# Performance work log

Measured on AMD Instinct MI355X. Metric: run time of the kernel, lower is better.

The kernel has to match this reference:

```python
import jax, jax.numpy as jnp
import numpy as np

N, E, EQ, DIM = 50000, 800000, 100000, 256


def setup_inputs() -> dict:
    key = jax.random.key(0)
    k1, k2, k3, k4, k5 = jax.random.split(key, 5)
    edges = jax.random.randint(k1, (2, EQ), 0, N)
    adj_row = jax.random.randint(k2, (E,), 0, N)
    adj_col = jax.random.randint(k3, (E,), 0, N)
    node_weight = jax.random.uniform(k4, (N,), dtype=jnp.float32)
    # torchhd-style bipolar hypervectors scaled by sqrt(1/dim)
    scale = (1.0 / DIM) ** 0.5
    node_vectors = jnp.sign(jax.random.normal(k5, (N, DIM), dtype=jnp.float32)) * scale
    return dict(edges=edges, adj_row=adj_row, adj_col=adj_col,
                node_weight=node_weight, node_vectors=node_vectors)


def reference(edges, adj_row, adj_col, node_weight, node_vectors):
    n = node_vectors.shape[0]
    # get_random_node_vectors: embedding * node_weight
    x = node_vectors * node_weight[:, None]                       # [N, dim]
    # one_hop_x = A @ x ; two_hop_x = A @ one_hop_x (binary adjacency)
    one_hop = jax.ops.segment_sum(x[adj_col], adj_row, num_segments=n)       # [N, dim]
    two_hop = jax.ops.segment_sum(one_hop[adj_col], adj_row, num_segments=n)  # [N, dim]
    deg = jax.ops.segment_sum(jnp.ones(adj_row.shape, x.dtype), adj_row, num_segments=n)  # [N]
    s, t = edges[0], edges[1]
    dot = lambda a, b: (a * b).sum(-1)
    count_1_1 = dot(one_hop[s], one_hop[t])
    count_1_2 = dot(one_hop[s], two_hop[t]) + dot(two_hop[s], one_hop[t])
    count_2_2 = dot(two_hop[s] - deg[s][:, None] * x[s],
                    two_hop[t] - deg[t][:, None] * x[t])
    count_self_1_2 = dot(one_hop[s], two_hop[s]) + dot(one_hop[t], two_hop[t])
    return (count_1_1, count_1_2, count_2_2, count_self_1_2)
```

## Files before the change

kernel.cpp:

```cpp
#include <hip/hip_runtime.h>

#define DIM 256
#define NODE_U2 192
#define NODE_U4 96
#define SLOT_OH_U4 32
#define SLOT_TH_U4 64

#define NSL 8
#define ECAP 2048

__device__ __forceinline__ unsigned int f2bf_rne(float f) {
    unsigned int u = __float_as_uint(f);
    return (u + 0x7fffu + ((u >> 16) & 1u)) >> 16;
}
__device__ __forceinline__ float bf_lo(unsigned int u) {
    return __uint_as_float(u << 16);
}
__device__ __forceinline__ float bf_hi(unsigned int u) {
    return __uint_as_float(u & 0xffff0000u);
}
__device__ __forceinline__ unsigned int pack2(float a, float b) {
    return f2bf_rne(a) | (f2bf_rne(b) << 16);
}

#define ACC8(v)                                            \
    do {                                                   \
        a0 += bf_lo((v).x); a1 += bf_hi((v).x);            \
        a2 += bf_lo((v).y); a3 += bf_hi((v).y);            \
        a4 += bf_lo((v).z); a5 += bf_hi((v).z);            \
        a6 += bf_lo((v).w); a7 += bf_hi((v).w);            \
    } while (0)

__global__ void x_kernel(const float* __restrict__ nv,
                         const float* __restrict__ w,
                         uint2* __restrict__ cmb,
                         uint2* __restrict__ xs_sl,
                         int total_u2, int N) {
    int i0 = blockIdx.x * blockDim.x + threadIdx.x;
    int stride = gridDim.x * blockDim.x;
    for (int i = i0; i < total_u2; i += stride) {
        float4 v = reinterpret_cast<const float4*>(nv)[i];
        int node = i >> 6;
        int j = i & 63;
        float wt = w[node];
        uint2 r;
        r.x = pack2(v.x * wt, v.y * wt);
        r.y = pack2(v.z * wt, v.w * wt);
        cmb[(size_t)node * NODE_U2 + j] = r;
        int s = j >> 3;
        xs_sl[((size_t)s * N + node) * 8 + (j & 7)] = r;
    }
}

__global__ void hist_kernel(const int* __restrict__ adj_row,
                            int* __restrict__ cnt, int E, int per_part) {
    int bp = blockIdx.x & 7;
    unsigned lo = (unsigned)(bp * per_part);
    int chunk = blockIdx.x >> 3;
    int nchunks = gridDim.x >> 3;
    int E4 = E >> 2;
    for (int i = chunk * 256 + threadIdx.x; i < E4; i += nchunks * 256) {
        int4 r4 = reinterpret_cast<const int4*>(adj_row)[i];
        if ((unsigned)(r4.x - lo) < (unsigned)per_part) atomicAdd(&cnt[r4.x], 1);
        if ((unsigned)(r4.y - lo) < (unsigned)per_part) atomicAdd(&cnt[r4.y], 1);
        if ((unsigned)(r4.z - lo) < (unsigned)per_part) atomicAdd(&cnt[r4.z], 1);
        if ((unsigned)(r4.w - lo) < (unsigned)per_part) atomicAdd(&cnt[r4.w], 1);
    }
    if (bp == 0 && chunk == 0) {
        for (int e = (E & ~3) + threadIdx.x; e < E; e += 256)
            atomicAdd(&cnt[adj_row[e]], 1);
    }
}

__global__ void block_sum_kernel(const int* __restrict__ in,
                                 int* __restrict__ sums, int n) {
    __shared__ int lds[256];
    int i = blockIdx.x * 256 + threadIdx.x;
    lds[threadIdx.x] = (i < n) ? in[i] : 0;
    __syncthreads();
    #pragma unroll
    for (int off = 128; off > 0; off >>= 1) {
        if (threadIdx.x < off) lds[threadIdx.x] += lds[threadIdx.x + off];
        __syncthreads();
    }
    if (threadIdx.x == 0) sums[blockIdx.x] = lds[0];
}

__global__ void scan_sums_kernel(int* __restrict__ sums, int nb,
                                 int* __restrict__ total_out) {
    __shared__ int lds[256];
    int v = (threadIdx.x < nb) ? sums[threadIdx.x] : 0;
    lds[threadIdx.x] = v;
    __syncthreads();
    #pragma unroll
    for (int off = 1; off < 256; off <<= 1) {
        int t = (threadIdx.x >= off) ? lds[threadIdx.x - off] : 0;
        __syncthreads();
        lds[threadIdx.x] += t;
        __syncthreads();
    }
    if (threadIdx.x < nb) sums[threadIdx.x] = lds[threadIdx.x] - v;
    if (threadIdx.x == 255) *total_out = lds[255];
}

__global__ void scan_block_kernel(const int* __restrict__ in,
                                  const int* __restrict__ sums,
                                  int* __restrict__ out1,
                                  int* __restrict__ out2, int n) {
    __shared__ int lds[256];
    int i = blockIdx.x * 256 + threadIdx.x;
    int v = (i < n) ? in[i] : 0;
    lds[threadIdx.x] = v;
    __syncthreads();
    #pragma unroll
    for (int off = 1; off < 256; off <<= 1) {
        int t = (threadIdx.x >= off) ? lds[threadIdx.x - off] : 0;
        __syncthreads();
        lds[threadIdx.x] += t;
        __syncthreads();
    }
    if (i < n) {
        int excl = sums[blockIdx.x] + lds[threadIdx.x] - v;
        out1[i] = excl;
        out2[i] = excl;
    }
}

__global__ void scatter_perm_part_kernel(const int* __restrict__ row,
                                         const int* __restrict__ col,
                                         int* __restrict__ cursor,
                                         unsigned short* __restrict__ perm,
                                         int E, int per_part) {
    int bp = blockIdx.x & 7;
    unsigned lo = (unsigned)(bp * per_part);
    int chunk = blockIdx.x >> 3;
    int nchunks = gridDim.x >> 3;
    int E4 = E >> 2;
    for (int i = chunk * 256 + threadIdx.x; i < E4; i += nchunks * 256) {
        int4 r4 = reinterpret_cast<const int4*>(row)[i];
        int e = i << 2;
        if ((unsigned)(r4.x - lo) < (unsigned)per_part) {
            int pos = atomicAdd(&cursor[r4.x], 1);
            perm[pos] = (unsigned short)col[e];
        }
        if ((unsigned)(r4.y - lo) < (unsigned)per_part) {
            int pos = atomicAdd(&cursor[r4.y], 1);
            perm[pos] = (unsigned short)col[e + 1];
        }
        if ((unsigned)(r4.z - lo) < (unsigned)per_part) {
            int pos = atomicAdd(&cursor[r4.z], 1);
            perm[pos] = (unsigned short)col[e + 2];
        }
        if ((unsigned)(r4.w - lo) < (unsigned)per_part) {
            int pos = atomicAdd(&cursor[r4.w], 1);
            perm[pos] = (unsigned short)col[e + 3];
        }
    }
    if (bp == 0 && chunk == 0) {
        for (int e = (E & ~3) + threadIdx.x; e < E; e += 256) {
            int pos = atomicAdd(&cursor[row[e]], 1);
            perm[pos] = (unsigned short)col[e];
        }
    }
}

__global__ void gather_sliced_kernel(const int* __restrict__ row_ptr,
                                     const unsigned short* __restrict__ perm,
                                     const uint4* __restrict__ src_sl,
                                     uint4* __restrict__ dst_sl,
                                     uint4* __restrict__ dst_cmb_slot,
                                     int N) {
    __shared__ unsigned short eidx[ECAP];
    int s = blockIdx.x & (NSL - 1);
    int rb = blockIdx.x >> 3;
    int r0 = rb * 64;
    int rlim = r0 + 64 < N ? r0 + 64 : N;
    int beg0 = row_ptr[r0];
    int end0 = row_ptr[rlim];
    int L = end0 - beg0;
    int Lc = L < ECAP ? L : ECAP;
    for (int i = threadIdx.x; i < Lc; i += 256) eidx[i] = perm[beg0 + i];
    __syncthreads();

    int g = threadIdx.x >> 2;
    int j = threadIdx.x & 3;
    int r = r0 + g;
    if (r >= N) return;

    int beg = row_ptr[r];
    int end = row_ptr[r + 1];
    const uint4* base = src_sl + (size_t)s * N * 4;

    float a0 = 0.f, a1 = 0.f, a2 = 0.f, a3 = 0.f;
    float a4 = 0.f, a5 = 0.f, a6 = 0.f, a7 = 0.f;

    if (end - beg0 <= ECAP) {
        int o = beg - beg0;
        int cnt = end - beg;
        int k = 0;
        for (; k + 3 < cnt; k += 4) {
            int c0 = eidx[o + k];
            int c1 = eidx[o + k + 1];
            int c2 = eidx[o + k + 2];
            int c3 = eidx[o + k + 3];
            uint4 v0 = base[(size_t)c0 * 4 + j];
            uint4 v1 = base[(size_t)c1 * 4 + j];
            uint4 v2 = base[(size_t)c2 * 4 + j];
            uint4 v3 = base[(size_t)c3 * 4 + j];
            ACC8(v0); ACC8(v1); ACC8(v2); ACC8(v3);
        }
        for (; k < cnt; ++k) {
            uint4 v = base[(size_t)eidx[o + k] * 4 + j];
            ACC8(v);
        }
    } else {
        for (int e = beg; e < end; ++e) {
            uint4 v = base[(size_t)perm[e] * 4 + j];
            ACC8(v);
        }
    }

    uint4 o4;
    o4.x = pack2(a0, a1);
    o4.y = pack2(a2, a3);
    o4.z = pack2(a4, a5);
    o4.w = pack2(a6, a7);
    if (dst_sl) dst_sl[((size_t)s * N + r) * 4 + j] = o4;
    dst_cmb_slot[(size_t)r * NODE_U4 + s * 4 + j] = o4;
}

__global__ void query_kernel(const int* __restrict__ es,
                             const int* __restrict__ et,
                             const uint4* __restrict__ cmb4,
                             const int* __restrict__ row_ptr,
                             float* __restrict__ out, int nq) {
    int gid = blockIdx.x * blockDim.x + threadIdx.x;
    int q = gid >> 5;
    if (q >= nq) return;
    int l = gid & 31;

    int s = es[q];
    int t = et[q];

    const uint4* ns = cmb4 + (size_t)s * NODE_U4;
    const uint4* nt = cmb4 + (size_t)t * NODE_U4;

    uint4 vxs = ns[l];
    uint4 vos = ns[SLOT_OH_U4 + l];
    uint4 vts = ns[SLOT_TH_U4 + l];
    uint4 vxt = nt[l];
    uint4 vot = nt[SLOT_OH_U4 + l];
    uint4 vtt = nt[SLOT_TH_U4 + l];
    float ds = (float)(row_ptr[s + 1] - row_ptr[s]);
    float dt = (float)(row_ptr[t + 1] - row_ptr[t]);

    float c11 = 0.f, c12 = 0.f, c22 = 0.f, cs = 0.f;
    const unsigned int* pxs = (const unsigned int*)&vxs;
    const unsigned int* pxt = (const unsigned int*)&vxt;
    const unsigned int* pos_ = (const unsigned int*)&vos;
    const unsigned int* pot = (const unsigned int*)&vot;
    const unsigned int* pts = (const unsigned int*)&vts;
    const unsigned int* ptt = (const unsigned int*)&vtt;
    #pragma unroll
    for (int k = 0; k < 4; ++k) {
        {
            float fxs = bf_lo(pxs[k]), fxt = bf_lo(pxt[k]);
            float fos = bf_lo(pos_[k]), fot = bf_lo(pot[k]);
            float fts = bf_lo(pts[k]), ftt = bf_lo(ptt[k]);
            c11 += fos * fot;
            c12 += fos * ftt + fts * fot;
            float as = fts - ds * fxs;
            float bt = ftt - dt * fxt;
            c22 += as * bt;
            cs  += fos * fts + fot * ftt;
        }
        {
            float fxs = bf_hi(pxs[k]), fxt = bf_hi(pxt[k]);
            float fos = bf_hi(pos_[k]), fot = bf_hi(pot[k]);
            float fts = bf_hi(pts[k]), ftt = bf_hi(ptt[k]);
            c11 += fos * fot;
            c12 += fos * ftt + fts * fot;
            float as = fts - ds * fxs;
            float bt = ftt - dt * fxt;
            c22 += as * bt;
            cs  += fos * fts + fot * ftt;
        }
    }

    #pragma unroll
    for (int off = 16; off > 0; off >>= 1) {
        c11 += __shfl_xor(c11, off);
        c12 += __shfl_xor(c12, off);
        c22 += __shfl_xor(c22, off);
        cs  += __shfl_xor(cs,  off);
    }

    if (l == 0) {
        out[q]          = c11;
        out[nq + q]     = c12;
        out[2 * nq + q] = c22;
        out[3 * nq + q] = cs;
    }
}

extern "C" void kernel_launch(void* const* d_in, const int* in_sizes, int n_in,
                              void* d_out, int out_size, void* d_ws, size_t ws_size,
                              hipStream_t stream) {
    const int*   edges        = (const int*)  d_in[0];
    const int*   adj_row      = (const int*)  d_in[1];
    const int*   adj_col      = (const int*)  d_in[2];
    const float* node_weight  = (const float*)d_in[3];
    const float* node_vectors = (const float*)d_in[4];

    const int EQ = in_sizes[0] / 2;
    const int E  = in_sizes[1];
    const int N  = in_sizes[3];

    uint2* cmb   = (uint2*)d_ws;
    uint2* xs_sl = cmb + (size_t)N * NODE_U2;
    uint2* oh_sl = xs_sl + (size_t)N * NSL * 8;
    int* row_ptr = (int*)(oh_sl + (size_t)N * NSL * 8);
    int* cursor  = row_ptr + (N + 1);
    int* cnt     = cursor + N;
    unsigned short* perm = (unsigned short*)(cnt + N);
    int* s1      = (int*)(perm + ((E + 1) & ~1));

    const int* es = edges;
    const int* et = edges + EQ;
    float* out = (float*)d_out;

    const int nb0 = (N + 255) / 256;
    const int per_part = (N + 7) / 8;

    hipMemsetAsync(cnt, 0, (size_t)N * sizeof(int), stream);
    int total_u2 = N * 64;
    x_kernel<<<2048, 256, 0, stream>>>(node_vectors, node_weight,
                                       cmb, xs_sl, total_u2, N);

    hist_kernel<<<2048, 256, 0, stream>>>(adj_row, cnt, E, per_part);

    block_sum_kernel<<<nb0, 256, 0, stream>>>(cnt, s1, N);
    scan_sums_kernel<<<1, 256, 0, stream>>>(s1, nb0, row_ptr + N);
    scan_block_kernel<<<nb0, 256, 0, stream>>>(cnt, s1, row_ptr, cursor, N);
    scatter_perm_part_kernel<<<2048, 256, 0, stream>>>(adj_row, adj_col,
                                                       cursor, perm, E,
                                                       per_part);

    const uint4* xs4 = (const uint4*)xs_sl;
    uint4* oh4 = (uint4*)oh_sl;
    uint4* cmb4 = (uint4*)cmb;
    int nrb = (N + 63) / 64;
    int gblocks = nrb * NSL;
    gather_sliced_kernel<<<gblocks, 256, 0, stream>>>(
        row_ptr, perm, xs4, oh4, cmb4 + SLOT_OH_U4, N);
    gather_sliced_kernel<<<gblocks, 256, 0, stream>>>(
        row_ptr, perm, (const uint4*)oh4, (uint4*)nullptr,
        cmb4 + SLOT_TH_U4, N);

    int qthreads = EQ * 32;
    query_kernel<<<(qthreads + 255) / 256, 256, 0, stream>>>(
        es, et, cmb4, row_ptr, out, EQ);
}
```

Baseline: 238.8 us.

## Sort rows by degree for load-balanced gather and fuse x with histogram

```diff
diff --git a/kernel.cpp b/kernel.cpp
--- a/kernel.cpp
+++ b/kernel.cpp
@@ -7,7 +7,8 @@
 #define SLOT_TH_U4 64
 
 #define NSL 8
-#define ECAP 2048
+#define ECAP 4096
+#define NBIN 64
 
 __device__ __forceinline__ unsigned int f2bf_rne(float f) {
     unsigned int u = __float_as_uint(f);
@@ -31,11 +32,13 @@
         a6 += bf_lo((v).w); a7 += bf_hi((v).w);            \
     } while (0)
 
-__global__ void x_kernel(const float* __restrict__ nv,
-                         const float* __restrict__ w,
-                         uint2* __restrict__ cmb,
-                         uint2* __restrict__ xs_sl,
-                         int total_u2, int N) {
+__global__ void x_and_hist_kernel(const float* __restrict__ nv,
+                                  const float* __restrict__ w,
+                                  uint2* __restrict__ cmb,
+                                  uint2* __restrict__ xs_sl,
+                                  int total_u2, int N,
+                                  const int* __restrict__ adj_row,
+                                  int* __restrict__ deg, int E, int per_part) {
     int i0 = blockIdx.x * blockDim.x + threadIdx.x;
     int stride = gridDim.x * blockDim.x;
     for (int i = i0; i < total_u2; i += stride) {
@@ -50,10 +53,6 @@
         int s = j >> 3;
         xs_sl[((size_t)s * N + node) * 8 + (j & 7)] = r;
     }
-}
-
-__global__ void hist_kernel(const int* __restrict__ adj_row,
-                            int* __restrict__ cnt, int E, int per_part) {
     int bp = blockIdx.x & 7;
     unsigned lo = (unsigned)(bp * per_part);
     int chunk = blockIdx.x >> 3;
@@ -61,14 +60,57 @@
     int E4 = E >> 2;
     for (int i = chunk * 256 + threadIdx.x; i < E4; i += nchunks * 256) {
         int4 r4 = reinterpret_cast<const int4*>(adj_row)[i];
-        if ((unsigned)(r4.x - lo) < (unsigned)per_part) atomicAdd(&cnt[r4.x], 1);
-        if ((unsigned)(r4.y - lo) < (unsigned)per_part) atomicAdd(&cnt[r4.y], 1);
-        if ((unsigned)(r4.z - lo) < (unsigned)per_part) atomicAdd(&cnt[r4.z], 1);
-        if ((unsigned)(r4.w - lo) < (unsigned)per_part) atomicAdd(&cnt[r4.w], 1);
+        if ((unsigned)(r4.x - lo) < (unsigned)per_part) atomicAdd(&deg[r4.x], 1);
+        if ((unsigned)(r4.y - lo) < (unsigned)per_part) atomicAdd(&deg[r4.y], 1);
+        if ((unsigned)(r4.z - lo) < (unsigned)per_part) atomicAdd(&deg[r4.z], 1);
+        if ((unsigned)(r4.w - lo) < (unsigned)per_part) atomicAdd(&deg[r4.w], 1);
     }
     if (bp == 0 && chunk == 0) {
         for (int e = (E & ~3) + threadIdx.x; e < E; e += 256)
-            atomicAdd(&cnt[adj_row[e]], 1);
+            atomicAdd(&deg[adj_row[e]], 1);
+    }
+}
+
+__global__ void bin_count_kernel(const int* __restrict__ deg,
+                                 int* __restrict__ blockBin, int n, int nblk) {
+    __shared__ int h[NBIN];
+    if (threadIdx.x < NBIN) h[threadIdx.x] = 0;
+    __syncthreads();
+    int i = blockIdx.x * 256 + threadIdx.x;
+    if (i < n) {
+        int b = deg[i]; b = b > NBIN - 1 ? NBIN - 1 : b;
+        atomicAdd(&h[b], 1);
+    }
+    __syncthreads();
+    if (threadIdx.x < NBIN)
+        blockBin[(size_t)threadIdx.x * nblk + blockIdx.x] = h[threadIdx.x];
+}
+
+__global__ void rank_assign_kernel(const int* __restrict__ deg,
+                                   const int* __restrict__ off,
+                                   int* __restrict__ rank2node,
+                                   int* __restrict__ node2rank,
+                                   int* __restrict__ degR, int n, int nblk) {
+    __shared__ int h[NBIN];
+    __shared__ int base[NBIN];
+    if (threadIdx.x < NBIN) h[threadIdx.x] = 0;
+    __syncthreads();
+    int i = blockIdx.x * 256 + threadIdx.x;
+    int b = 0, loc = 0, d = 0;
+    bool act = i < n;
+    if (act) {
+        d = deg[i]; b = d > NBIN - 1 ? NBIN - 1 : d;
+        loc = atomicAdd(&h[b], 1);
+    }
+    __syncthreads();
+    if (threadIdx.x < NBIN)
+        base[threadIdx.x] = off[(size_t)threadIdx.x * nblk + blockIdx.x];
+    __syncthreads();
+    if (act) {
+        int r = base[b] + loc;
+        rank2node[r] = i;
+        node2rank[i] = r;
+        degR[r] = d;
     }
 }
 
@@ -128,6 +170,7 @@
 
 __global__ void scatter_perm_part_kernel(const int* __restrict__ row,
                                          const int* __restrict__ col,
+                                         const int* __restrict__ node2rank,
                                          int* __restrict__ cursor,
                                          unsigned short* __restrict__ perm,
                                          int E, int per_part) {
@@ -139,26 +182,31 @@
     for (int i = chunk * 256 + threadIdx.x; i < E4; i += nchunks * 256) {
         int4 r4 = reinterpret_cast<const int4*>(row)[i];
         int e = i << 2;
-        if ((unsigned)(r4.x - lo) < (unsigned)per_part) {
-            int pos = atomicAdd(&cursor[r4.x], 1);
+        int k0 = node2rank[r4.x];
+        int k1 = node2rank[r4.y];
+        int k2 = node2rank[r4.z];
+        int k3 = node2rank[r4.w];
+        if ((unsigned)(k0 - lo) < (unsigned)per_part) {
+            int pos = atomicAdd(&cursor[k0], 1);
             perm[pos] = (unsigned short)col[e];
         }
-        if ((unsigned)(r4.y - lo) < (unsigned)per_part) {
-            int pos = atomicAdd(&cursor[r4.y], 1);
+        if ((unsigned)(k1 - lo) < (unsigned)per_part) {
+            int pos = atomicAdd(&cursor[k1], 1);
             perm[pos] = (unsigned short)col[e + 1];
         }
-        if ((unsigned)(r4.z - lo) < (unsigned)per_part) {
-            int pos = atomicAdd(&cursor[r4.z], 1);
+        if ((unsigned)(k2 - lo) < (unsigned)per_part) {
+            int pos = atomicAdd(&cursor[k2], 1);
             perm[pos] = (unsigned short)col[e + 2];
         }
-        if ((unsigned)(r4.w - lo) < (unsigned)per_part) {
-            int pos = atomicAdd(&cursor[r4.w], 1);
+        if ((unsigned)(k3 - lo) < (unsigned)per_part) {
+            int pos = atomicAdd(&cursor[k3], 1);
             perm[pos] = (unsigned short)col[e + 3];
         }
     }
     if (bp == 0 && chunk == 0) {
         for (int e = (E & ~3) + threadIdx.x; e < E; e += 256) {
-            int pos = atomicAdd(&cursor[row[e]], 1);
+            int k = node2rank[row[e]];
+            int pos = atomicAdd(&cursor[k], 1);
             perm[pos] = (unsigned short)col[e];
         }
     }
@@ -166,6 +214,7 @@
 
 __global__ void gather_sliced_kernel(const int* __restrict__ row_ptr,
                                      const unsigned short* __restrict__ perm,
+                                     const int* __restrict__ rank2node,
                                      const uint4* __restrict__ src_sl,
                                      uint4* __restrict__ dst_sl,
                                      uint4* __restrict__ dst_cmb_slot,
@@ -187,6 +236,7 @@
     int r = r0 + g;
     if (r >= N) return;
 
+    int node = rank2node[r];
     int beg = row_ptr[r];
     int end = row_ptr[r + 1];
     const uint4* base = src_sl + (size_t)s * N * 4;
@@ -194,7 +244,7 @@
     float a0 = 0.f, a1 = 0.f, a2 = 0.f, a3 = 0.f;
     float a4 = 0.f, a5 = 0.f, a6 = 0.f, a7 = 0.f;
 
-    if (end - beg0 <= ECAP) {
+    if (L <= ECAP) {
         int o = beg - beg0;
         int cnt = end - beg;
         int k = 0;
@@ -225,14 +275,14 @@
     o4.y = pack2(a2, a3);
     o4.z = pack2(a4, a5);
     o4.w = pack2(a6, a7);
-    if (dst_sl) dst_sl[((size_t)s * N + r) * 4 + j] = o4;
-    dst_cmb_slot[(size_t)r * NODE_U4 + s * 4 + j] = o4;
+    if (dst_sl) dst_sl[((size_t)s * N + node) * 4 + j] = o4;
+    dst_cmb_slot[(size_t)node * NODE_U4 + s * 4 + j] = o4;
 }
 
 __global__ void query_kernel(const int* __restrict__ es,
                              const int* __restrict__ et,
                              const uint4* __restrict__ cmb4,
-                             const int* __restrict__ row_ptr,
+                             const int* __restrict__ deg,
                              float* __restrict__ out, int nq) {
     int gid = blockIdx.x * blockDim.x + threadIdx.x;
     int q = gid >> 5;
@@ -251,8 +301,8 @@
     uint4 vxt = nt[l];
     uint4 vot = nt[SLOT_OH_U4 + l];
     uint4 vtt = nt[SLOT_TH_U4 + l];
-    float ds = (float)(row_ptr[s + 1] - row_ptr[s]);
-    float dt = (float)(row_ptr[t + 1] - row_ptr[t]);
+    float ds = (float)deg[s];
+    float dt = (float)deg[t];
 
     float c11 = 0.f, c12 = 0.f, c22 = 0.f, cs = 0.f;
     const unsigned int* pxs = (const unsigned int*)&vxs;
@@ -316,35 +366,50 @@
     const int E  = in_sizes[1];
     const int N  = in_sizes[3];
 
+    const int nbB = (N + 255) / 256;
+    const int n1  = NBIN * nbB;
+    const int nbS = (n1 + 255) / 256;
+
     uint2* cmb   = (uint2*)d_ws;
     uint2* xs_sl = cmb + (size_t)N * NODE_U2;
-    uint2* oh_sl = xs_sl + (size_t)N * NSL * 8;
-    int* row_ptr = (int*)(oh_sl + (size_t)N * NSL * 8);
-    int* cursor  = row_ptr + (N + 1);
-    int* cnt     = cursor + N;
-    unsigned short* perm = (unsigned short*)(cnt + N);
-    int* s1      = (int*)(perm + ((E + 1) & ~1));
+    uint2* oh_sl = xs_sl + (size_t)N * 64;
+    int* deg      = (int*)(oh_sl + (size_t)N * 64);
+    int* node2rank = deg + N;
+    int* rank2node = node2rank + N;
+    int* degR     = rank2node + N;
+    int* row_ptr  = degR + N;
+    int* cursor   = row_ptr + (N + 1);
+    int* blockBin = cursor + N;
+    int* s1       = blockBin + n1;
+    unsigned short* perm = (unsigned short*)(s1 + 256);
 
     const int* es = edges;
     const int* et = edges + EQ;
     float* out = (float*)d_out;
 
-    const int nb0 = (N + 255) / 256;
-    const int per_part = (N + 7) / 8;
-
-    hipMemsetAsync(cnt, 0, (size_t)N * sizeof(int), stream);
+    const int per_part_node = (N + 7) / 8;
+    const int per_part_rank = (N + 7) / 8;
+
+    hipMemsetAsync(deg, 0, (size_t)N * sizeof(int), stream);
     int total_u2 = N * 64;
-    x_kernel<<<2048, 256, 0, stream>>>(node_vectors, node_weight,
-                                       cmb, xs_sl, total_u2, N);
-
-    hist_kernel<<<2048, 256, 0, stream>>>(adj_row, cnt, E, per_part);
-
-    block_sum_kernel<<<nb0, 256, 0, stream>>>(cnt, s1, N);
-    scan_sums_kernel<<<1, 256, 0, stream>>>(s1, nb0, row_ptr + N);
-    scan_block_kernel<<<nb0, 256, 0, stream>>>(cnt, s1, row_ptr, cursor, N);
+    x_and_hist_kernel<<<2048, 256, 0, stream>>>(node_vectors, node_weight,
+                                                cmb, xs_sl, total_u2, N,
+                                                adj_row, deg, E, per_part_node);
+
+    bin_count_kernel<<<nbB, 256, 0, stream>>>(deg, blockBin, N, nbB);
+    block_sum_kernel<<<nbS, 256, 0, stream>>>(blockBin, s1, n1);
+    scan_sums_kernel<<<1, 256, 0, stream>>>(s1, nbS, cursor );
+    scan_block_kernel<<<nbS, 256, 0, stream>>>(blockBin, s1, blockBin,
+                                               blockBin, n1);
+    rank_assign_kernel<<<nbB, 256, 0, stream>>>(deg, blockBin, rank2node,
+                                                node2rank, degR, N, nbB);
+
+    block_sum_kernel<<<nbB, 256, 0, stream>>>(degR, s1, N);
+    scan_sums_kernel<<<1, 256, 0, stream>>>(s1, nbB, row_ptr + N);
+    scan_block_kernel<<<nbB, 256, 0, stream>>>(degR, s1, row_ptr, cursor, N);
     scatter_perm_part_kernel<<<2048, 256, 0, stream>>>(adj_row, adj_col,
-                                                       cursor, perm, E,
-                                                       per_part);
+                                                       node2rank, cursor, perm,
+                                                       E, per_part_rank);
 
     const uint4* xs4 = (const uint4*)xs_sl;
     uint4* oh4 = (uint4*)oh_sl;
@@ -352,12 +417,12 @@
     int nrb = (N + 63) / 64;
     int gblocks = nrb * NSL;
     gather_sliced_kernel<<<gblocks, 256, 0, stream>>>(
-        row_ptr, perm, xs4, oh4, cmb4 + SLOT_OH_U4, N);
+        row_ptr, perm, rank2node, xs4, oh4, cmb4 + SLOT_OH_U4, N);
     gather_sliced_kernel<<<gblocks, 256, 0, stream>>>(
-        row_ptr, perm, (const uint4*)oh4, (uint4*)nullptr,
+        row_ptr, perm, rank2node, (const uint4*)oh4, (uint4*)nullptr,
         cmb4 + SLOT_TH_U4, N);
 
     int qthreads = EQ * 32;
     query_kernel<<<(qthreads + 255) / 256, 256, 0, stream>>>(
-        es, et, cmb4, row_ptr, out, EQ);
-}
+        es, et, cmb4, deg, out, EQ);
+}
```

Measured after the change: 244.5 us. 2.4% more time.

## Sort queries by source node and fuse histogram into x kernel

Applied to the files above, without the earlier changes.

```diff
diff --git a/kernel.cpp b/kernel.cpp
--- a/kernel.cpp
+++ b/kernel.cpp
@@ -31,11 +31,16 @@
         a6 += bf_lo((v).w); a7 += bf_hi((v).w);            \
     } while (0)
 
-__global__ void x_kernel(const float* __restrict__ nv,
-                         const float* __restrict__ w,
-                         uint2* __restrict__ cmb,
-                         uint2* __restrict__ xs_sl,
-                         int total_u2, int N) {
+__global__ void x_and_hist_kernel(const float* __restrict__ nv,
+                                  const float* __restrict__ w,
+                                  uint2* __restrict__ cmb,
+                                  uint2* __restrict__ xs_sl,
+                                  int total_u2, int N,
+                                  const int* __restrict__ adj_row,
+                                  int* __restrict__ cnt, int E,
+                                  const int* __restrict__ es,
+                                  int* __restrict__ qcnt, int EQ,
+                                  int per_part) {
     int i0 = blockIdx.x * blockDim.x + threadIdx.x;
     int stride = gridDim.x * blockDim.x;
     for (int i = i0; i < total_u2; i += stride) {
@@ -50,10 +55,6 @@
         int s = j >> 3;
         xs_sl[((size_t)s * N + node) * 8 + (j & 7)] = r;
     }
-}
-
-__global__ void hist_kernel(const int* __restrict__ adj_row,
-                            int* __restrict__ cnt, int E, int per_part) {
     int bp = blockIdx.x & 7;
     unsigned lo = (unsigned)(bp * per_part);
     int chunk = blockIdx.x >> 3;
@@ -66,9 +67,19 @@
         if ((unsigned)(r4.z - lo) < (unsigned)per_part) atomicAdd(&cnt[r4.z], 1);
         if ((unsigned)(r4.w - lo) < (unsigned)per_part) atomicAdd(&cnt[r4.w], 1);
     }
+    int Q4 = EQ >> 2;
+    for (int i = chunk * 256 + threadIdx.x; i < Q4; i += nchunks * 256) {
+        int4 s4 = reinterpret_cast<const int4*>(es)[i];
+        if ((unsigned)(s4.x - lo) < (unsigned)per_part) atomicAdd(&qcnt[s4.x], 1);
+        if ((unsigned)(s4.y - lo) < (unsigned)per_part) atomicAdd(&qcnt[s4.y], 1);
+        if ((unsigned)(s4.z - lo) < (unsigned)per_part) atomicAdd(&qcnt[s4.z], 1);
+        if ((unsigned)(s4.w - lo) < (unsigned)per_part) atomicAdd(&qcnt[s4.w], 1);
+    }
     if (bp == 0 && chunk == 0) {
         for (int e = (E & ~3) + threadIdx.x; e < E; e += 256)
             atomicAdd(&cnt[adj_row[e]], 1);
+        for (int q = (EQ & ~3) + threadIdx.x; q < EQ; q += 256)
+            atomicAdd(&qcnt[es[q]], 1);
     }
 }
 
@@ -160,6 +171,48 @@
         for (int e = (E & ~3) + threadIdx.x; e < E; e += 256) {
             int pos = atomicAdd(&cursor[row[e]], 1);
             perm[pos] = (unsigned short)col[e];
+        }
+    }
+}
+
+__global__ void qscatter_part_kernel(const int* __restrict__ es,
+                                     const int* __restrict__ et,
+                                     int* __restrict__ qcur,
+                                     int* __restrict__ qs,
+                                     int* __restrict__ qt,
+                                     int* __restrict__ qidx,
+                                     int EQ, int per_part) {
+    int bp = blockIdx.x & 7;
+    unsigned lo = (unsigned)(bp * per_part);
+    int chunk = blockIdx.x >> 3;
+    int nchunks = gridDim.x >> 3;
+    int Q4 = EQ >> 2;
+    for (int i = chunk * 256 + threadIdx.x; i < Q4; i += nchunks * 256) {
+        int4 s4 = reinterpret_cast<const int4*>(es)[i];
+        int4 t4 = reinterpret_cast<const int4*>(et)[i];
+        int q = i << 2;
+        if ((unsigned)(s4.x - lo) < (unsigned)per_part) {
+            int pos = atomicAdd(&qcur[s4.x], 1);
+            qs[pos] = s4.x; qt[pos] = t4.x; qidx[pos] = q;
+        }
+        if ((unsigned)(s4.y - lo) < (unsigned)per_part) {
+            int pos = atomicAdd(&qcur[s4.y], 1);
+            qs[pos] = s4.y; qt[pos] = t4.y; qidx[pos] = q + 1;
+        }
+        if ((unsigned)(s4.z - lo) < (unsigned)per_part) {
+            int pos = atomicAdd(&qcur[s4.z], 1);
+            qs[pos] = s4.z; qt[pos] = t4.z; qidx[pos] = q + 2;
+        }
+        if ((unsigned)(s4.w - lo) < (unsigned)per_part) {
+            int pos = atomicAdd(&qcur[s4.w], 1);
+            qs[pos] = s4.w; qt[pos] = t4.w; qidx[pos] = q + 3;
+        }
+    }
+    if (bp == 0 && chunk == 0) {
+        for (int q = (EQ & ~3) + threadIdx.x; q < EQ; q += 256) {
+            int s = es[q];
+            int pos = atomicAdd(&qcur[s], 1);
+            qs[pos] = s; qt[pos] = et[q]; qidx[pos] = q;
         }
     }
 }
@@ -194,7 +247,7 @@
     float a0 = 0.f, a1 = 0.f, a2 = 0.f, a3 = 0.f;
     float a4 = 0.f, a5 = 0.f, a6 = 0.f, a7 = 0.f;
 
-    if (end - beg0 <= ECAP) {
+    if (L <= ECAP) {
         int o = beg - beg0;
         int cnt = end - beg;
         int k = 0;
@@ -229,18 +282,20 @@
     dst_cmb_slot[(size_t)r * NODE_U4 + s * 4 + j] = o4;
 }
 
-__global__ void query_kernel(const int* __restrict__ es,
-                             const int* __restrict__ et,
+__global__ void query_kernel(const int* __restrict__ qs,
+                             const int* __restrict__ qt,
+                             const int* __restrict__ qidx,
                              const uint4* __restrict__ cmb4,
-                             const int* __restrict__ row_ptr,
+                             const int* __restrict__ deg,
                              float* __restrict__ out, int nq) {
     int gid = blockIdx.x * blockDim.x + threadIdx.x;
     int q = gid >> 5;
     if (q >= nq) return;
     int l = gid & 31;
 
-    int s = es[q];
-    int t = et[q];
+    int s = qs[q];
+    int t = qt[q];
+    int oq = qidx[q];
 
     const uint4* ns = cmb4 + (size_t)s * NODE_U4;
     const uint4* nt = cmb4 + (size_t)t * NODE_U4;
@@ -251,8 +306,8 @@
     uint4 vxt = nt[l];
     uint4 vot = nt[SLOT_OH_U4 + l];
     uint4 vtt = nt[SLOT_TH_U4 + l];
-    float ds = (float)(row_ptr[s + 1] - row_ptr[s]);
-    float dt = (float)(row_ptr[t + 1] - row_ptr[t]);
+    float ds = (float)deg[s];
+    float dt = (float)deg[t];
 
     float c11 = 0.f, c12 = 0.f, c22 = 0.f, cs = 0.f;
     const unsigned int* pxs = (const unsigned int*)&vxs;
@@ -296,10 +351,10 @@
     }
 
     if (l == 0) {
-        out[q]          = c11;
-        out[nq + q]     = c12;
-        out[2 * nq + q] = c22;
-        out[3 * nq + q] = cs;
+        out[oq]          = c11;
+        out[nq + oq]     = c12;
+        out[2 * nq + oq] = c22;
+        out[3 * nq + oq] = cs;
     }
 }
 
@@ -318,12 +373,17 @@
 
     uint2* cmb   = (uint2*)d_ws;
     uint2* xs_sl = cmb + (size_t)N * NODE_U2;
-    uint2* oh_sl = xs_sl + (size_t)N * NSL * 8;
-    int* row_ptr = (int*)(oh_sl + (size_t)N * NSL * 8);
+    uint2* oh_sl = xs_sl + (size_t)N * 64;
+    int* row_ptr = (int*)(oh_sl + (size_t)N * 64);
     int* cursor  = row_ptr + (N + 1);
     int* cnt     = cursor + N;
-    unsigned short* perm = (unsigned short*)(cnt + N);
-    int* s1      = (int*)(perm + ((E + 1) & ~1));
+    int* qcnt    = cnt + N;
+    int* qcur    = qcnt + N;
+    int* qs      = qcur + N;
+    int* qt      = qs + EQ;
+    int* qidx    = qt + EQ;
+    int* s1      = qidx + EQ;
+    unsigned short* perm = (unsigned short*)(s1 + 256);
 
     const int* es = edges;
     const int* et = edges + EQ;
@@ -332,12 +392,12 @@
     const int nb0 = (N + 255) / 256;
     const int per_part = (N + 7) / 8;
 
-    hipMemsetAsync(cnt, 0, (size_t)N * sizeof(int), stream);
+    hipMemsetAsync(cnt, 0, (size_t)2 * N * sizeof(int), stream);
     int total_u2 = N * 64;
-    x_kernel<<<2048, 256, 0, stream>>>(node_vectors, node_weight,
-                                       cmb, xs_sl, total_u2, N);
-
-    hist_kernel<<<2048, 256, 0, stream>>>(adj_row, cnt, E, per_part);
+    x_and_hist_kernel<<<2048, 256, 0, stream>>>(node_vectors, node_weight,
+                                                cmb, xs_sl, total_u2, N,
+                                                adj_row, cnt, E,
+                                                es, qcnt, EQ, per_part);
 
     block_sum_kernel<<<nb0, 256, 0, stream>>>(cnt, s1, N);
     scan_sums_kernel<<<1, 256, 0, stream>>>(s1, nb0, row_ptr + N);
@@ -345,6 +405,12 @@
     scatter_perm_part_kernel<<<2048, 256, 0, stream>>>(adj_row, adj_col,
                                                        cursor, perm, E,
                                                        per_part);
+
+    block_sum_kernel<<<nb0, 256, 0, stream>>>(qcnt, s1, N);
+    scan_sums_kernel<<<1, 256, 0, stream>>>(s1, nb0, s1 + 250);
+    scan_block_kernel<<<nb0, 256, 0, stream>>>(qcnt, s1, qcnt, qcur, N);
+    qscatter_part_kernel<<<2048, 256, 0, stream>>>(es, et, qcur, qs, qt, qidx,
+                                                   EQ, per_part);
 
     const uint4* xs4 = (const uint4*)xs_sl;
     uint4* oh4 = (uint4*)oh_sl;
@@ -359,5 +425,5 @@
 
     int qthreads = EQ * 32;
     query_kernel<<<(qthreads + 255) / 256, 256, 0, stream>>>(
-        es, et, cmb4, row_ptr, out, EQ);
-}
+        qs, qt, qidx, cmb4, cnt, out, EQ);
+}
```

After: 243.7 us. 1.02x slower.
